# Performance work log

Measured on AMD Instinct MI355X. Metric: run time of the kernel, lower is better.

Reference implementation:

```python
import jax, jax.numpy as jnp
import numpy as np

D_MODEL, N_HEADS, E_LAYERS, D_FF, FACTOR, REP = 128, 8, 5, 64, 3, 128


def setup_inputs() -> dict:
    key = jax.random.key(0)
    ks = jax.random.split(key, 8)
    B, L = 8, 4096
    s = 0.02
    E = E_LAYERS
    def p(k, shape):
        return jax.random.normal(k, shape, jnp.float32) * s
    return dict(
        x=jax.random.normal(ks[0], (B, D_MODEL, L), jnp.float32),
        Wq=p(ks[1], (E, D_MODEL, D_MODEL)), bq=jnp.zeros((E, D_MODEL), jnp.float32),
        Wk=p(ks[2], (E, D_MODEL, D_MODEL)), bk=jnp.zeros((E, D_MODEL), jnp.float32),
        Wv=p(ks[3], (E, D_MODEL, D_MODEL)), bv=jnp.zeros((E, D_MODEL), jnp.float32),
        Wo=p(ks[4], (E, D_MODEL, D_MODEL)), bo=jnp.zeros((E, D_MODEL), jnp.float32),
        W1=p(ks[5], (E, D_FF, D_MODEL)), b1=jnp.zeros((E, D_FF), jnp.float32),
        W2=p(ks[6], (E, D_MODEL, D_FF)), b2=jnp.zeros((E, D_MODEL), jnp.float32),
        ln1_w=jnp.ones((E, D_MODEL), jnp.float32), ln1_b=jnp.zeros((E, D_MODEL), jnp.float32),
        ln2_w=jnp.ones((E, D_MODEL), jnp.float32), ln2_b=jnp.zeros((E, D_MODEL), jnp.float32),
        lnf_w=jnp.ones((D_MODEL,), jnp.float32), lnf_b=jnp.zeros((D_MODEL,), jnp.float32),
        Wp=p(ks[7], (D_MODEL, REP)), bp=jnp.zeros((REP,), jnp.float32),
    )


def _ln(x, w, b, eps=1e-5):
    m = jnp.mean(x, axis=-1, keepdims=True)
    v = jnp.mean((x - m) ** 2, axis=-1, keepdims=True)
    return (x - m) * jax.lax.rsqrt(v + eps) * w + b


def _prob_attn(Q, K, V, key):
    """ProbSparse self-attention (mask_flag=False). Q,K,V: [B,H,L,Eh]."""
    B, H, L, Eh = Q.shape
    c = min(int(FACTOR * np.ceil(np.log(L))), L)  # U_part == u for self-attn
    # sample c keys per query position (shared across batch/head, like torch.randint)
    idx = jax.random.randint(key, (L, c), 0, L)
    Ks = K[:, :, idx, :]                                   # [B,H,L,c,Eh]
    QKs = jnp.einsum('bhle,bhlue->bhlu', Q, Ks)            # sampled scores
    M = QKs.max(-1) - QKs.sum(-1) / L                      # sparsity measure [B,H,L]
    _, top = jax.lax.top_k(M, c)                           # top-u query indices [B,H,c]
    Qr = jnp.take_along_axis(Q, top[..., None], axis=2)    # [B,H,c,Eh]
    scores = jnp.einsum('bhue,bhke->bhuk', Qr, K) * (1.0 / np.sqrt(Eh))
    attn = jax.nn.softmax(scores, axis=-1)                 # [B,H,c,L]
    upd = jnp.einsum('bhuk,bhke->bhue', attn, V)           # [B,H,c,Eh]
    # lazy context: mean of V for non-selected queries
    ctx = jnp.broadcast_to(V.mean(axis=2, keepdims=True), Q.shape)
    bi = jnp.arange(B)[:, None, None]
    hi = jnp.arange(H)[None, :, None]
    ctx = ctx.at[bi, hi, top].set(upd)
    return ctx


def reference(x, Wq, bq, Wk, bk, Wv, bv, Wo, bo, W1, b1, W2, b2,
              ln1_w, ln1_b, ln2_w, ln2_b, lnf_w, lnf_b, Wp, bp):
    B, _, L = x.shape
    Eh = D_MODEL // N_HEADS
    h = jnp.transpose(x, (0, 2, 1))                        # [B,L,D]
    base = jax.random.key(42)
    for l in range(E_LAYERS):
        q = (h @ Wq[l].T + bq[l]).reshape(B, L, N_HEADS, Eh).transpose(0, 2, 1, 3)
        k = (h @ Wk[l].T + bk[l]).reshape(B, L, N_HEADS, Eh).transpose(0, 2, 1, 3)
        v = (h @ Wv[l].T + bv[l]).reshape(B, L, N_HEADS, Eh).transpose(0, 2, 1, 3)
        ctx = _prob_attn(q, k, v, jax.random.fold_in(base, l))
        ctx = ctx.transpose(0, 2, 1, 3).reshape(B, L, D_MODEL)
        h = h + (ctx @ Wo[l].T + bo[l])                    # residual (dropout off)
        h = _ln(h, ln1_w[l], ln1_b[l])
        # 1x1 conv FFN == per-token linear
        y = jax.nn.gelu(h @ W1[l].T + b1[l], approximate=False)
        y = y @ W2[l].T + b2[l]
        h = _ln(h + y, ln2_w[l], ln2_b[l])
    h = _ln(h, lnf_w, lnf_b)
    out = h @ Wp + bp                                      # [B,L,REP]
    return jnp.transpose(out, (0, 2, 1))                   # [B,REP,L]
```

## Files before the change

### kernel.cpp

```cpp
#include <hip/hip_runtime.h>
#include <stdint.h>
#include <math.h>

#define DM   128
#define NH   8
#define EHD  16
#define NLAY 5
#define DFF  64
#define NREP 128
#define NB   8
#define SL   4096
#define NC   27
#define NBH  (NB*NH)
#define NROWS (NB*SL)
#define ACH  4

typedef _Float16 f16;
typedef f16 f16x8 __attribute__((ext_vector_type(8)));
typedef float f32x16 __attribute__((ext_vector_type(16)));

__device__ __forceinline__ uint32_t rotl32(uint32_t v, int d) {
  return (v << d) | (v >> (32 - d));
}

__device__ __forceinline__ void tf2x32(uint32_t k0, uint32_t k1,
                                       uint32_t x0, uint32_t x1,
                                       uint32_t &o0, uint32_t &o1) {
  uint32_t ks2 = k0 ^ k1 ^ 0x1BD11BDAu;
  x0 += k0; x1 += k1;
#define TFR(r) { x0 += x1; x1 = rotl32(x1, (r)); x1 ^= x0; }
  TFR(13) TFR(15) TFR(26) TFR(6)
  x0 += k1; x1 += ks2 + 1u;
  TFR(17) TFR(29) TFR(16) TFR(24)
  x0 += ks2; x1 += k0 + 2u;
  TFR(13) TFR(15) TFR(26) TFR(6)
  x0 += k0; x1 += k1 + 3u;
  TFR(17) TFR(29) TFR(16) TFR(24)
  x0 += k1; x1 += ks2 + 4u;
  TFR(13) TFR(15) TFR(26) TFR(6)
  x0 += ks2; x1 += k0 + 5u;
#undef TFR
  o0 = x0; o1 = x1;
}

__global__ void gen_bits_kernel(uint32_t* __restrict__ bits, int layer) {
  int i = blockIdx.x * blockDim.x + threadIdx.x;
  if (i >= SL * NC) return;
  uint32_t ka, kb, k2a, k2b, y0, y1;
  tf2x32(0u, 42u, 0u, (uint32_t)layer, ka, kb);
  tf2x32(ka, kb, 0u, 1u, k2a, k2b);
  tf2x32(k2a, k2b, 0u, (uint32_t)i, y0, y1);
  bits[i] = y0 ^ y1;
}

__global__ __launch_bounds__(256) void transpose_x_kernel(const float* __restrict__ x,
                                                          float* __restrict__ h) {
  __shared__ float t[32][33];
  int tid = threadIdx.x;
  int tx = tid & 31, ty = tid >> 5;
  int l0 = blockIdx.x * 32, d0 = blockIdx.y * 32, b = blockIdx.z;
#pragma unroll
  for (int j = 0; j < 4; ++j) {
    int d = d0 + ty + 8 * j;
    t[ty + 8 * j][tx] = x[((size_t)b * DM + d) * SL + l0 + tx];
  }
  __syncthreads();
#pragma unroll
  for (int j = 0; j < 4; ++j) {
    int l = l0 + ty + 8 * j;
    h[((size_t)b * SL + l) * DM + d0 + tx] = t[tx][ty + 8 * j];
  }
}

#define PACK_TOTAL 425984
__global__ __launch_bounds__(256) void prep_weights(
    const float* __restrict__ Wq, const float* __restrict__ Wk,
    const float* __restrict__ Wv, const float* __restrict__ Wo,
    const float* __restrict__ W1, const float* __restrict__ W2,
    const float* __restrict__ Wp, f16* __restrict__ phi) {
  int idx = blockIdx.x * 256 + threadIdx.x;
  if (idx >= PACK_TOTAL) return;
  const float* src; int K, KS16, lsh; int f; bool transp = false;
  if (idx >= 409600) { f = idx - 409600; src = Wp; K = 128; KS16 = 8; lsh = 3; transp = true; }
  else {
    int layer = idx / 81920; int r = idx - layer * 81920;
    if      (r < 16384) { src = Wq + layer * 16384; f = r;         K = 128; KS16 = 8; lsh = 3; }
    else if (r < 32768) { src = Wk + layer * 16384; f = r - 16384; K = 128; KS16 = 8; lsh = 3; }
    else if (r < 49152) { src = Wv + layer * 16384; f = r - 32768; K = 128; KS16 = 8; lsh = 3; }
    else if (r < 65536) { src = Wo + layer * 16384; f = r - 49152; K = 128; KS16 = 8; lsh = 3; }
    else if (r < 73728) { src = W1 + layer * 8192;  f = r - 65536; K = 128; KS16 = 8; lsh = 3; }
    else                { src = W2 + layer * 8192;  f = r - 73728; K = 64;  KS16 = 4; lsh = 2; }
  }
  int j = f & 7, lane = (f >> 3) & 63, rest = f >> 9;
  int ks = rest & (KS16 - 1), nt = rest >> lsh;
  int n = nt * 32 + (lane & 31);
  int kk = ks * 16 + ((lane >> 5) & 1) * 8 + j;
  float x = transp ? src[(size_t)kk * 128 + n] : src[(size_t)n * K + kk];
  phi[idx] = (f16)x;
}

template<int NT32, int KS16, int SRC, int EPI>
__global__ __launch_bounds__(256, 2) void gemm_fused(
    const float* __restrict__ Asrc, const f16* __restrict__ phi,
    const float* __restrict__ bias0, const float* __restrict__ bias1,
    const float* __restrict__ bias2,
    float* out0, float* out1, float* out2,
    const float* __restrict__ gw, const float* __restrict__ gb,
    const float* hres) {
  constexpr int NGW = NT32 / 2;
  constexpr int K = KS16 * 16;
  __shared__ f16x8 Alds[2 * 2 * KS16 * 64];
  __shared__ f16x8 Blds[NT32 * KS16 * 64];
  __shared__ float red[64 * 4];
  int tid = threadIdx.x, lane = tid & 63, wid = tid >> 6;
  int mg = wid >> 1, ng = wid & 1;
  int row0 = blockIdx.x * 64;

  if constexpr (SRC == 0 || SRC == 1) {
    constexpr int OCT = 64 * (K / 8);
    for (int o = tid; o < OCT; o += 256) {
      int row = o / (K / 8);
      int k0 = (o % (K / 8)) * 8;
      float4 f0, f1;
      if constexpr (SRC == 0) {
        const float* s = Asrc + (size_t)(row0 + row) * K + k0;
        f0 = *(const float4*)(s);
        f1 = *(const float4*)(s + 4);
      } else {
        int gr = row0 + row; int bb = gr >> 12, ll = gr & (SL - 1);
        int head = k0 >> 4, e0 = k0 & 15;
        const float* s = Asrc + (((size_t)(bb * NH + head) * SL + ll) * EHD + e0);
        f0 = *(const float4*)(s);
        f1 = *(const float4*)(s + 4);
      }
      f16x8 vh, vl;
      float xs[8] = {f0.x, f0.y, f0.z, f0.w, f1.x, f1.y, f1.z, f1.w};
#pragma unroll
      for (int j = 0; j < 8; ++j) {
        f16 hh = (f16)xs[j];
        vh[j] = hh;
        vl[j] = (f16)(xs[j] - (float)hh);
      }
      int al = (row & 31) | (((k0 >> 3) & 1) << 5);
      int ks = k0 >> 4, mt = row >> 5;
      Alds[((0 * 2 + mt) * KS16 + ks) * 64 + al] = vh;
      Alds[((1 * 2 + mt) * KS16 + ks) * 64 + al] = vl;
    }
  } else {
    int row = tid >> 2, q4 = tid & 3;
    const float* s = Asrc + (size_t)(row0 + row) * 128 + q4 * 32;
    float r[32];
#pragma unroll
    for (int i = 0; i < 8; ++i) {
      float4 f = *(const float4*)(s + 4 * i);
      r[4 * i] = f.x; r[4 * i + 1] = f.y; r[4 * i + 2] = f.z; r[4 * i + 3] = f.w;
    }
    float sm = 0.f, s2 = 0.f;
#pragma unroll
    for (int i = 0; i < 32; ++i) { sm += r[i]; s2 += r[i] * r[i]; }
    sm += __shfl_xor(sm, 1, 4); sm += __shfl_xor(sm, 2, 4);
    s2 += __shfl_xor(s2, 1, 4); s2 += __shfl_xor(s2, 2, 4);
    float mean = sm * (1.f / 128.f);
    float var = s2 * (1.f / 128.f) - mean * mean;
    float rstd = 1.0f / sqrtf(var + 1e-5f);
#pragma unroll
    for (int i = 0; i < 32; ++i) {
      int kk = q4 * 32 + i;
      r[i] = (r[i] - mean) * rstd * gw[kk] + gb[kk];
    }
#pragma unroll
    for (int i = 0; i < 4; ++i) {
      int k0 = q4 * 32 + i * 8;
      f16x8 vh, vl;
#pragma unroll
      for (int j = 0; j < 8; ++j) {
        float x = r[8 * i + j];
        f16 hh = (f16)x;
        vh[j] = hh;
        vl[j] = (f16)(x - (float)hh);
      }
      int al = (row & 31) | (((k0 >> 3) & 1) << 5);
      int ks = k0 >> 4, mt = row >> 5;
      Alds[((0 * 2 + mt) * KS16 + ks) * 64 + al] = vh;
      Alds[((1 * 2 + mt) * KS16 + ks) * 64 + al] = vl;
    }
  }

  constexpr int NMAT = (EPI == 0) ? 3 : 1;
  constexpr int BCNT = NT32 * KS16 * 64;

#define STAGE_B(SRCPTR)                                        \
  {                                                            \
    const float4* bsrc = (const float4*)(SRCPTR);              \
    float4* bdst = (float4*)Blds;                              \
    _Pragma("unroll")                                          \
    for (int i = 0; i < BCNT / 256; ++i) bdst[tid + i * 256] = bsrc[tid + i * 256]; \
  }

#define GEMM_PASS(ASEL)                                                         \
  _Pragma("unroll")                                                             \
  for (int ks = 0; ks < KS16; ++ks) {                                           \
    f16x8 afr = Alds[(((ASEL) * 2 + mg) * KS16 + ks) * 64 + lane];              \
    _Pragma("unroll")                                                           \
    for (int g = 0; g < NGW; ++g) {                                             \
      f16x8 bfr = Blds[((ng * NGW + g) * KS16 + ks) * 64 + lane];               \
      acc[g] = __builtin_amdgcn_mfma_f32_32x32x16_f16(afr, bfr, acc[g], 0, 0, 0); \
    }                                                                           \
  }

  for (int m = 0; m < NMAT; ++m) {
    if (m) __syncthreads();
    STAGE_B(phi + m * 16384)
    __syncthreads();
    f32x16 acc[NGW];
#pragma unroll
    for (int g = 0; g < NGW; ++g)
#pragma unroll
      for (int j = 0; j < 16; ++j) acc[g][j] = 0.f;
    GEMM_PASS(0)
    GEMM_PASS(1)

    int hi4 = 4 * (lane >> 5);
    if constexpr (EPI == 0) {
      const float* bm = (m == 0) ? bias0 : (m == 1) ? bias1 : bias2;
      float* om = (m == 0) ? out0 : (m == 1) ? out1 : out2;
#pragma unroll
      for (int g = 0; g < NGW; ++g) {
        int col = ng * (NGW * 32) + g * 32 + (lane & 31);
        float bv = bm[col];
        int head = col >> 4, e = col & 15;
#pragma unroll
        for (int reg = 0; reg < 16; ++reg) {
          int row_l = (reg & 3) + 8 * (reg >> 2) + hi4;
          int grow = row0 + mg * 32 + row_l;
          int bb = grow >> 12, ll = grow & (SL - 1);
          om[((size_t)(bb * NH + head) * SL + ll) * EHD + e] = acc[g][reg] + bv;
        }
      }
    } else if constexpr (EPI == 3) {
#pragma unroll
      for (int g = 0; g < NGW; ++g) {
        int col = ng * (NGW * 32) + g * 32 + (lane & 31);
        float bv = bias0[col];
#pragma unroll
        for (int reg = 0; reg < 16; ++reg) {
          int row_l = (reg & 3) + 8 * (reg >> 2) + hi4;
          int grow = row0 + mg * 32 + row_l;
          int bb = grow >> 12, ll = grow & (SL - 1);
          out0[((size_t)(bb * NREP + col)) * SL + ll] = acc[g][reg] + bv;
        }
      }
    } else {
      float bv[2], gwv[2], gbv[2];
#pragma unroll
      for (int g = 0; g < NGW; ++g) {
        int col = ng * (NGW * 32) + g * 32 + (lane & 31);
        bv[g] = bias0[col]; gwv[g] = gw[col]; gbv[g] = gb[col];
      }
      float ps[16], pq[16];
#pragma unroll
      for (int reg = 0; reg < 16; ++reg) {
        int row_l = (reg & 3) + 8 * (reg >> 2) + hi4;
        int grow = row0 + mg * 32 + row_l;
        float vsum = 0.f, qsum = 0.f;
#pragma unroll
        for (int g = 0; g < NGW; ++g) {
          int col = ng * (NGW * 32) + g * 32 + (lane & 31);
          float t = acc[g][reg] + bv[g] + hres[(size_t)grow * DM + col];
          acc[g][reg] = t;
          vsum += t; qsum += t * t;
        }
        vsum += __shfl_xor(vsum, 1, 32); qsum += __shfl_xor(qsum, 1, 32);
        vsum += __shfl_xor(vsum, 2, 32); qsum += __shfl_xor(qsum, 2, 32);
        vsum += __shfl_xor(vsum, 4, 32); qsum += __shfl_xor(qsum, 4, 32);
        vsum += __shfl_xor(vsum, 8, 32); qsum += __shfl_xor(qsum, 8, 32);
        vsum += __shfl_xor(vsum, 16, 32); qsum += __shfl_xor(qsum, 16, 32);
        ps[reg] = vsum; pq[reg] = qsum;
      }
      __syncthreads();
      if ((lane & 31) == 0) {
#pragma unroll
        for (int reg = 0; reg < 16; ++reg) {
          int row_l = (reg & 3) + 8 * (reg >> 2) + hi4;
          int rl = mg * 32 + row_l;
          red[rl * 4 + ng * 2 + 0] = ps[reg];
          red[rl * 4 + ng * 2 + 1] = pq[reg];
        }
      }
      __syncthreads();
#pragma unroll
      for (int reg = 0; reg < 16; ++reg) {
        int row_l = (reg & 3) + 8 * (reg >> 2) + hi4;
        int rl = mg * 32 + row_l;
        int grow = row0 + rl;
        float st = red[rl * 4 + 0] + red[rl * 4 + 2];
        float qt = red[rl * 4 + 1] + red[rl * 4 + 3];
        float mean = st * (1.f / 128.f);
        float var = qt * (1.f / 128.f) - mean * mean;
        float rstd = 1.0f / sqrtf(var + 1e-5f);
#pragma unroll
        for (int g = 0; g < NGW; ++g) {
          int col = ng * (NGW * 32) + g * 32 + (lane & 31);
          out0[(size_t)grow * DM + col] = (acc[g][reg] - mean) * rstd * gwv[g] + gbv[g];
        }
      }
    }
  }
#undef STAGE_B
#undef GEMM_PASS
}

__global__ __launch_bounds__(256, 2) void gemm_ffn(
    const float* __restrict__ h,
    const f16* __restrict__ w1hi, const f16* __restrict__ w2hi,
    const float* __restrict__ b1, const float* __restrict__ b2,
    const float* __restrict__ gw, const float* __restrict__ gb,
    float* __restrict__ hout) {
  __shared__ f16x8 AldsH[2 * 2 * 8 * 64];
  __shared__ f16x8 Blds1[2 * 8 * 64];
  __shared__ float ybuf[64 * 64];
  __shared__ float red[64 * 4];
  f16x8* Alds2 = AldsH;
  f16x8* Blds2 = AldsH + 1024;
  int tid = threadIdx.x, lane = tid & 63, wid = tid >> 6;
  int mg = wid >> 1, ng = wid & 1;
  int row0 = blockIdx.x * 64;
  int hi4 = 4 * (lane >> 5);

  for (int o = tid; o < 64 * 16; o += 256) {
    int row = o >> 4;
    int k0 = (o & 15) * 8;
    const float* s = h + (size_t)(row0 + row) * 128 + k0;
    float4 f0 = *(const float4*)(s);
    float4 f1 = *(const float4*)(s + 4);
    f16x8 vh, vl;
    float xs[8] = {f0.x, f0.y, f0.z, f0.w, f1.x, f1.y, f1.z, f1.w};
#pragma unroll
    for (int j = 0; j < 8; ++j) {
      f16 hh = (f16)xs[j];
      vh[j] = hh;
      vl[j] = (f16)(xs[j] - (float)hh);
    }
    int al = (row & 31) | (((k0 >> 3) & 1) << 5);
    int ks = k0 >> 4, mt = row >> 5;
    AldsH[((0 * 2 + mt) * 8 + ks) * 64 + al] = vh;
    AldsH[((1 * 2 + mt) * 8 + ks) * 64 + al] = vl;
  }
  {
    const float4* bsrc = (const float4*)w1hi;
    float4* bdst = (float4*)Blds1;
#pragma unroll
    for (int i = 0; i < 4; ++i) bdst[tid + i * 256] = bsrc[tid + i * 256];
  }
  __syncthreads();
  f32x16 acc1;
#pragma unroll
  for (int j = 0; j < 16; ++j) acc1[j] = 0.f;
#pragma unroll
  for (int asel = 0; asel < 2; ++asel)
#pragma unroll
    for (int ks = 0; ks < 8; ++ks) {
      f16x8 afr = AldsH[((asel * 2 + mg) * 8 + ks) * 64 + lane];
      f16x8 bfr = Blds1[(ng * 8 + ks) * 64 + lane];
      acc1 = __builtin_amdgcn_mfma_f32_32x32x16_f16(afr, bfr, acc1, 0, 0, 0);
    }
  {
    int col = ng * 32 + (lane & 31);
    float bv = b1[col];
    const float is2 = 0.707106781186547524f;
#pragma unroll
    for (int reg = 0; reg < 16; ++reg) {
      int row_l = (reg & 3) + 8 * (reg >> 2) + hi4 + mg * 32;
      float a = acc1[reg] + bv;
      ybuf[row_l * 64 + col] = 0.5f * a * (1.f + erff(a * is2));
    }
  }
  __syncthreads();
  for (int o = tid; o < 64 * 8; o += 256) {
    int row = o >> 3;
    int k0 = (o & 7) * 8;
    f16x8 vh, vl;
#pragma unroll
    for (int j = 0; j < 8; ++j) {
      float x = ybuf[row * 64 + k0 + j];
      f16 hh = (f16)x;
      vh[j] = hh;
      vl[j] = (f16)(x - (float)hh);
    }
    int al = (row & 31) | (((k0 >> 3) & 1) << 5);
    int ks = k0 >> 4, mt = row >> 5;
    Alds2[((0 * 2 + mt) * 4 + ks) * 64 + al] = vh;
    Alds2[((1 * 2 + mt) * 4 + ks) * 64 + al] = vl;
  }
  {
    const float4* bsrc = (const float4*)w2hi;
    float4* bdst = (float4*)Blds2;
#pragma unroll
    for (int i = 0; i < 4; ++i) bdst[tid + i * 256] = bsrc[tid + i * 256];
  }
  __syncthreads();
  f32x16 acc[2];
#pragma unroll
  for (int g = 0; g < 2; ++g)
#pragma unroll
    for (int j = 0; j < 16; ++j) acc[g][j] = 0.f;
#pragma unroll
  for (int asel = 0; asel < 2; ++asel)
#pragma unroll
    for (int ks = 0; ks < 4; ++ks) {
      f16x8 afr = Alds2[((asel * 2 + mg) * 4 + ks) * 64 + lane];
#pragma unroll
      for (int g = 0; g < 2; ++g) {
        f16x8 bfr = Blds2[((ng * 2 + g) * 4 + ks) * 64 + lane];
        acc[g] = __builtin_amdgcn_mfma_f32_32x32x16_f16(afr, bfr, acc[g], 0, 0, 0);
      }
    }
  {
    float bv[2], gwv[2], gbv[2];
#pragma unroll
    for (int g = 0; g < 2; ++g) {
      int col = ng * 64 + g * 32 + (lane & 31);
      bv[g] = b2[col]; gwv[g] = gw[col]; gbv[g] = gb[col];
    }
    float ps[16], pq[16];
#pragma unroll
    for (int reg = 0; reg < 16; ++reg) {
      int row_l = (reg & 3) + 8 * (reg >> 2) + hi4;
      int grow = row0 + mg * 32 + row_l;
      float vsum = 0.f, qsum = 0.f;
#pragma unroll
      for (int g = 0; g < 2; ++g) {
        int col = ng * 64 + g * 32 + (lane & 31);
        float t = acc[g][reg] + bv[g] + h[(size_t)grow * DM + col];
        acc[g][reg] = t;
        vsum += t; qsum += t * t;
      }
      vsum += __shfl_xor(vsum, 1, 32); qsum += __shfl_xor(qsum, 1, 32);
      vsum += __shfl_xor(vsum, 2, 32); qsum += __shfl_xor(qsum, 2, 32);
      vsum += __shfl_xor(vsum, 4, 32); qsum += __shfl_xor(qsum, 4, 32);
      vsum += __shfl_xor(vsum, 8, 32); qsum += __shfl_xor(qsum, 8, 32);
      vsum += __shfl_xor(vsum, 16, 32); qsum += __shfl_xor(qsum, 16, 32);
      ps[reg] = vsum; pq[reg] = qsum;
    }
    __syncthreads();
    if ((lane & 31) == 0) {
#pragma unroll
      for (int reg = 0; reg < 16; ++reg) {
        int row_l = (reg & 3) + 8 * (reg >> 2) + hi4;
        int rl = mg * 32 + row_l;
        red[rl * 4 + ng * 2 + 0] = ps[reg];
        red[rl * 4 + ng * 2 + 1] = pq[reg];
      }
    }
    __syncthreads();
#pragma unroll
    for (int reg = 0; reg < 16; ++reg) {
      int row_l = (reg & 3) + 8 * (reg >> 2) + hi4;
      int rl = mg * 32 + row_l;
      int grow = row0 + rl;
      float st = red[rl * 4 + 0] + red[rl * 4 + 2];
      float qt = red[rl * 4 + 1] + red[rl * 4 + 3];
      float mean = st * (1.f / 128.f);
      float var = qt * (1.f / 128.f) - mean * mean;
      float rstd = 1.0f / sqrtf(var + 1e-5f);
#pragma unroll
      for (int g = 0; g < 2; ++g) {
        int col = ng * 64 + g * 32 + (lane & 31);
        hout[(size_t)grow * DM + col] = (acc[g][reg] - mean) * rstd * gwv[g] + gbv[g];
      }
    }
  }
}

__global__ __launch_bounds__(256) void sampM_kernel(const float* __restrict__ q,
    const float* __restrict__ k, const uint32_t* __restrict__ bits,
    float* __restrict__ M) {
  int tid = threadIdx.x;
  int wave = tid >> 6, lane = tid & 63;
  int bh = blockIdx.x & 63;
  int l = (blockIdx.x >> 6) * 4 + wave;
  int u = lane >> 1;
  bool act = (u < NC);
  int uc = act ? u : 0;
  int ki = (int)(bits[l * NC + uc] & (SL - 1));
  int h8 = (lane & 1) * 8;
  const float* kr = k + ((size_t)bh * SL + ki) * EHD + h8;
  float4 k0 = *(const float4*)(kr);
  float4 k1 = *(const float4*)(kr + 4);
  const float* qr = q + ((size_t)bh * SL + l) * EHD + h8;
  float4 q0 = *(const float4*)(qr);
  float4 q1 = *(const float4*)(qr + 4);
  float s = q0.x*k0.x + q0.y*k0.y + q0.z*k0.z + q0.w*k0.w
          + q1.x*k1.x + q1.y*k1.y + q1.z*k1.z + q1.w*k1.w;
  s += __shfl_xor(s, 1, 64);
  float mval = act ? s : -INFINITY;
  float sval = (act && (lane & 1) == 0) ? s : 0.f;
#pragma unroll
  for (int off = 2; off < 64; off <<= 1) {
    mval = fmaxf(mval, __shfl_xor(mval, off, 64));
    sval += __shfl_xor(sval, off, 64);
  }
  if (lane == 0) M[(size_t)bh * SL + l] = mval - sval * (1.0f / (float)SL);
}

__global__ __launch_bounds__(256) void topk_kernel(const float* __restrict__ M,
                                                   int* __restrict__ top) {
  int bh  = blockIdx.x;
  int tid = threadIdx.x;
  int lane = tid & 63, wave = tid >> 6;
  __shared__ float vals[SL];
  __shared__ float wmax[4];
  __shared__ int   widx[4];
  for (int i = tid; i < SL; i += 256) vals[i] = M[(size_t)bh * SL + i];
  __syncthreads();
  for (int u = 0; u < NC; ++u) {
    float bm = -INFINITY; int bi = SL;
#pragma unroll
    for (int j = 0; j < SL / 256; ++j) {
      int i = tid + j * 256;
      float vv = vals[i];
      if (vv > bm) { bm = vv; bi = i; }
    }
#pragma unroll
    for (int off = 32; off > 0; off >>= 1) {
      float v2 = __shfl_xor(bm, off, 64);
      int   i2 = __shfl_xor(bi, off, 64);
      if (v2 > bm || (v2 == bm && i2 < bi)) { bm = v2; bi = i2; }
    }
    if (lane == 0) { wmax[wave] = bm; widx[wave] = bi; }
    __syncthreads();
    if (tid == 0) {
      float b0 = wmax[0]; int x0 = widx[0];
#pragma unroll
      for (int w = 1; w < 4; ++w) {
        float vw = wmax[w]; int iw = widx[w];
        if (vw > b0 || (vw == b0 && iw < x0)) { b0 = vw; x0 = iw; }
      }
      top[bh * NC + u] = x0;
      vals[x0] = -INFINITY;
    }
    __syncthreads();
  }
}

__global__ __launch_bounds__(256) void vmean_part(const float* __restrict__ v,
                                                  float* __restrict__ partial) {
  int bh = blockIdx.x & 63;
  int chunk = blockIdx.x >> 6;
  int tid = threadIdx.x;
  int e = tid & 15, g = tid >> 4;
  const float* vb = v + ((size_t)bh * SL + chunk * 256) * EHD;
  float s = 0.f;
#pragma unroll
  for (int j = 0; j < 16; ++j) s += vb[(size_t)(j * 16 + g) * EHD + e];
  __shared__ float red[256];
  red[tid] = s; __syncthreads();
  for (int st = 128; st >= 16; st >>= 1) {
    if (tid < st) red[tid] += red[tid + st];
    __syncthreads();
  }
  if (tid < EHD) partial[(bh * 16 + chunk) * EHD + tid] = red[tid];
}

__global__ __launch_bounds__(256) void fillctx_kernel(const float* __restrict__ partial,
                                                      float* __restrict__ ctx) {
  __shared__ float vm[EHD];
  int tid = threadIdx.x;
  int t0 = blockIdx.x * 256;
  int bh = t0 >> 14;
  if (tid < EHD) {
    float s = 0.f;
#pragma unroll
    for (int c = 0; c < 16; ++c) s += partial[(bh * 16 + c) * EHD + tid];
    vm[tid] = s * (1.0f / (float)SL);
  }
  __syncthreads();
  int t = t0 + tid;
  int e0 = (t & 3) * 4;
  *(float4*)(ctx + (size_t)t * 4) = make_float4(vm[e0], vm[e0 + 1], vm[e0 + 2], vm[e0 + 3]);
}

__global__ __launch_bounds__(256) void attn_flash(const float* __restrict__ q,
    const float* __restrict__ k, const float* __restrict__ v,
    const int* __restrict__ top, float* __restrict__ pa) {
  int bh = blockIdx.x & 63, ug = (blockIdx.x >> 6) & 3, chunk = blockIdx.x >> 8;
  int tid = threadIdx.x, wid = tid >> 6, lane = tid & 63;
  int base = ug * 7;
  int nq = (ug < 3) ? 7 : 6;
  bool has0 = (wid < nq);
  bool has1 = (wid + 4 < nq);
  int u0 = base + (has0 ? wid : 0);
  int u1 = base + (has1 ? wid + 4 : 0);
  int qi0 = top[bh * NC + u0];
  int qi1 = top[bh * NC + u1];
  float q0[16], q1[16];
  {
    const float* p0 = q + ((size_t)bh * SL + qi0) * EHD;
    const float* p1 = q + ((size_t)bh * SL + qi1) * EHD;
#pragma unroll
    for (int i = 0; i < 4; ++i) {
      float4 f = *(const float4*)(p0 + 4 * i);
      q0[4*i] = f.x; q0[4*i+1] = f.y; q0[4*i+2] = f.z; q0[4*i+3] = f.w;
      float4 g = *(const float4*)(p1 + 4 * i);
      q1[4*i] = g.x; q1[4*i+1] = g.y; q1[4*i+2] = g.z; q1[4*i+3] = g.w;
    }
  }
  float m0 = -INFINITY, m1 = -INFINITY, l0 = 0.f, l1 = 0.f;
  float a0[16], a1[16];
#pragma unroll
  for (int j = 0; j < 16; ++j) { a0[j] = 0.f; a1[j] = 0.f; }
  const float* kb = k + (size_t)bh * SL * EHD;
  const float* vb = v + (size_t)bh * SL * EHD;
  int row_base = chunk * (SL / ACH);
  for (int t = 0; t < SL / ACH / 64; ++t) {
    int ki = row_base + lane + (t << 6);
    float kr[16], vr[16];
    {
      const float* kp = kb + (size_t)ki * EHD;
      const float* vp = vb + (size_t)ki * EHD;
#pragma unroll
      for (int i = 0; i < 4; ++i) {
        float4 f = *(const float4*)(kp + 4 * i);
        kr[4*i] = f.x; kr[4*i+1] = f.y; kr[4*i+2] = f.z; kr[4*i+3] = f.w;
        float4 g = *(const float4*)(vp + 4 * i);
        vr[4*i] = g.x; vr[4*i+1] = g.y; vr[4*i+2] = g.z; vr[4*i+3] = g.w;
      }
    }
    float s0 = 0.f, s1 = 0.f;
#pragma unroll
    for (int j = 0; j < 16; ++j) { s0 += q0[j] * kr[j]; s1 += q1[j] * kr[j]; }
    s0 *= 0.25f; s1 *= 0.25f;
    {
      float d = s0 - m0;
      float e = expf(-fabsf(d));
      bool gt = d > 0.f;
      float c = gt ? e : 1.f;
      float p = gt ? 1.f : e;
      m0 = gt ? s0 : m0;
      l0 = l0 * c + p;
#pragma unroll
      for (int j = 0; j < 16; ++j) a0[j] = a0[j] * c + p * vr[j];
    }
    {
      float d = s1 - m1;
      float e = expf(-fabsf(d));
      bool gt = d > 0.f;
      float c = gt ? e : 1.f;
      float p = gt ? 1.f : e;
      m1 = gt ? s1 : m1;
      l1 = l1 * c + p;
#pragma unroll
      for (int j = 0; j < 16; ++j) a1[j] = a1[j] * c + p * vr[j];
    }
  }
#pragma unroll
  for (int off = 1; off < 64; off <<= 1) {
    {
      float mo = __shfl_xor(m0, off, 64);
      float lo_ = __shfl_xor(l0, off, 64);
      float mn = fmaxf(m0, mo);
      float cs = expf(m0 - mn), co = expf(mo - mn);
      l0 = l0 * cs + lo_ * co;
#pragma unroll
      for (int j = 0; j < 16; ++j) {
        float ao = __shfl_xor(a0[j], off, 64);
        a0[j] = a0[j] * cs + ao * co;
      }
      m0 = mn;
    }
    {
      float mo = __shfl_xor(m1, off, 64);
      float lo_ = __shfl_xor(l1, off, 64);
      float mn = fmaxf(m1, mo);
      float cs = expf(m1 - mn), co = expf(mo - mn);
      l1 = l1 * cs + lo_ * co;
#pragma unroll
      for (int j = 0; j < 16; ++j) {
        float ao = __shfl_xor(a1[j], off, 64);
        a1[j] = a1[j] * cs + ao * co;
      }
      m1 = mn;
    }
  }
  if (lane == 0 && has0) {
    float* o = pa + ((size_t)(bh * NC + u0) * ACH + chunk) * 18;
    o[0] = m0; o[1] = l0;
#pragma unroll
    for (int j = 0; j < 16; ++j) o[2 + j] = a0[j];
  }
  if (lane == 0 && has1) {
    float* o = pa + ((size_t)(bh * NC + u1) * ACH + chunk) * 18;
    o[0] = m1; o[1] = l1;
#pragma unroll
    for (int j = 0; j < 16; ++j) o[2 + j] = a1[j];
  }
}

__global__ __launch_bounds__(64) void attn_merge(const float* __restrict__ pa,
    const int* __restrict__ top, float* __restrict__ ctx) {
  int bh = blockIdx.x;
  int u = threadIdx.x;
  if (u >= NC) return;
  float m = -INFINITY, L = 0.f;
  float a[16];
#pragma unroll
  for (int j = 0; j < 16; ++j) a[j] = 0.f;
#pragma unroll
  for (int c = 0; c < ACH; ++c) {
    const float* p = pa + ((size_t)(bh * NC + u) * ACH + c) * 18;
    float pm = p[0], pl = p[1];
    float mn = fmaxf(m, pm);
    float cs = expf(m - mn), co = expf(pm - mn);
    L = L * cs + pl * co;
#pragma unroll
    for (int j = 0; j < 16; ++j) a[j] = a[j] * cs + p[2 + j] * co;
    m = mn;
  }
  int qi = top[bh * NC + u];
  float inv = 1.0f / L;
  float* o = ctx + ((size_t)bh * SL + qi) * EHD;
#pragma unroll
  for (int j = 0; j < 16; ++j) o[j] = a[j] * inv;
}

extern "C" void kernel_launch(void* const* d_in, const int* in_sizes, int n_in,
                              void* d_out, int out_size, void* d_ws, size_t ws_size,
                              hipStream_t stream) {
  const float* x   = (const float*)d_in[0];
  const float* Wq  = (const float*)d_in[1];
  const float* bq  = (const float*)d_in[2];
  const float* Wk  = (const float*)d_in[3];
  const float* bk  = (const float*)d_in[4];
  const float* Wv  = (const float*)d_in[5];
  const float* bv  = (const float*)d_in[6];
  const float* Wo  = (const float*)d_in[7];
  const float* bo  = (const float*)d_in[8];
  const float* W1  = (const float*)d_in[9];
  const float* b1  = (const float*)d_in[10];
  const float* W2  = (const float*)d_in[11];
  const float* b2  = (const float*)d_in[12];
  const float* ln1w = (const float*)d_in[13];
  const float* ln1b = (const float*)d_in[14];
  const float* ln2w = (const float*)d_in[15];
  const float* ln2b = (const float*)d_in[16];
  const float* lnfw = (const float*)d_in[17];
  const float* lnfb = (const float*)d_in[18];
  const float* Wp  = (const float*)d_in[19];
  const float* bp  = (const float*)d_in[20];
  float* out = (float*)d_out;

  float* ws = (float*)d_ws;
  float* h     = ws;
  float* q     = ws + 4194304;
  float* k     = ws + 8388608;
  float* v     = ws + 12582912;
  float* ctx   = ws + 16777216;
  float* partial = ws + 20971520;
  float* pa    = ws + 20987904;
  float* M     = ws + 23068672;
  int*   top   = (int*)(ws + 23331840);
  uint32_t* bits = (uint32_t*)(ws + 23333888);
  f16* phi = (f16*)(ws + 23444480);

  transpose_x_kernel<<<dim3(SL / 32, DM / 32, NB), 256, 0, stream>>>(x, h);
  prep_weights<<<(PACK_TOTAL + 255) / 256, 256, 0, stream>>>(
      Wq, Wk, Wv, Wo, W1, W2, Wp, phi);

  for (int l = 0; l < NLAY; ++l) {
    size_t lb = (size_t)l * 81920;
    gen_bits_kernel<<<(SL * NC + 255) / 256, 256, 0, stream>>>(bits, l);
    gemm_fused<4, 8, 0, 0><<<NROWS / 64, 256, 0, stream>>>(
        h, phi + lb, bq + l * DM, bk + l * DM, bv + l * DM,
        q, k, v, nullptr, nullptr, nullptr);
    sampM_kernel<<<NBH * SL / 4, 256, 0, stream>>>(q, k, bits, M);
    topk_kernel<<<NBH, 256, 0, stream>>>(M, top);
    vmean_part<<<NBH * 16, 256, 0, stream>>>(v, partial);
    fillctx_kernel<<<NBH * SL * 4 / 256, 256, 0, stream>>>(partial, ctx);
    attn_flash<<<ACH * 256, 256, 0, stream>>>(q, k, v, top, pa);
    attn_merge<<<NBH, 64, 0, stream>>>(pa, top, ctx);
    gemm_fused<4, 8, 1, 1><<<NROWS / 64, 256, 0, stream>>>(
        ctx, phi + lb + 49152, bo + l * DM, nullptr, nullptr,
        h, nullptr, nullptr, ln1w + l * DM, ln1b + l * DM, h);
    gemm_ffn<<<NROWS / 64, 256, 0, stream>>>(
        h, phi + lb + 65536, phi + lb + 73728,
        b1 + l * DFF, b2 + l * DM, ln2w + l * DM, ln2b + l * DM, h);
  }

  gemm_fused<4, 8, 3, 3><<<NROWS / 64, 256, 0, stream>>>(
      h, phi + 409600, bp, nullptr, nullptr,
      out, nullptr, nullptr, lnfw, lnfb, nullptr);
}
```

Before: 941.1 us.

## Store Q and a K copy position-major so sampling reads all heads coalesced

Result: slower. 986.5 us (+4.8%).

```diff
diff --git a/kernel.cpp b/kernel.cpp
--- a/kernel.cpp
+++ b/kernel.cpp
@@ -104,7 +104,7 @@
     const float* __restrict__ Asrc, const f16* __restrict__ phi,
     const float* __restrict__ bias0, const float* __restrict__ bias1,
     const float* __restrict__ bias2,
-    float* out0, float* out1, float* out2,
+    float* out0, float* out1, float* out2, float* out3,
     const float* __restrict__ gw, const float* __restrict__ gb,
     const float* hres) {
   constexpr int NGW = NT32 / 2;
@@ -234,7 +234,14 @@
           int row_l = (reg & 3) + 8 * (reg >> 2) + hi4;
           int grow = row0 + mg * 32 + row_l;
           int bb = grow >> 12, ll = grow & (SL - 1);
-          om[((size_t)(bb * NH + head) * SL + ll) * EHD + e] = acc[g][reg] + bv;
+          float val = acc[g][reg] + bv;
+          if (m == 0) {
+            om[((size_t)ll * NBH + bb * NH + head) * EHD + e] = val;
+          } else {
+            om[((size_t)(bb * NH + head) * SL + ll) * EHD + e] = val;
+            if (m == 1)
+              out3[((size_t)ll * NBH + bb * NH + head) * EHD + e] = val;
+          }
         }
       }
     } else if constexpr (EPI == 3) {
@@ -472,35 +479,55 @@
   }
 }
 
-__global__ __launch_bounds__(256) void sampM_kernel(const float* __restrict__ q,
-    const float* __restrict__ k, const uint32_t* __restrict__ bits,
+__global__ __launch_bounds__(256) void sampM_kernel(const float* __restrict__ qt,
+    const float* __restrict__ kt, const uint32_t* __restrict__ bits,
     float* __restrict__ M) {
+  __shared__ float smx[4][64];
+  __shared__ float ssm[4][64];
   int tid = threadIdx.x;
-  int wave = tid >> 6, lane = tid & 63;
-  int bh = blockIdx.x & 63;
-  int l = (blockIdx.x >> 6) * 4 + wave;
-  int u = lane >> 1;
-  bool act = (u < NC);
-  int uc = act ? u : 0;
-  int ki = (int)(bits[l * NC + uc] & (SL - 1));
-  int h8 = (lane & 1) * 8;
-  const float* kr = k + ((size_t)bh * SL + ki) * EHD + h8;
-  float4 k0 = *(const float4*)(kr);
-  float4 k1 = *(const float4*)(kr + 4);
-  const float* qr = q + ((size_t)bh * SL + l) * EHD + h8;
-  float4 q0 = *(const float4*)(qr);
+  int uslot = tid >> 6, bh = tid & 63;
+  int l = blockIdx.x;
+  const float* qr = qt + ((size_t)l * NBH + bh) * EHD;
+  float4 q0 = *(const float4*)(qr + 0);
   float4 q1 = *(const float4*)(qr + 4);
-  float s = q0.x*k0.x + q0.y*k0.y + q0.z*k0.z + q0.w*k0.w
-          + q1.x*k1.x + q1.y*k1.y + q1.z*k1.z + q1.w*k1.w;
-  s += __shfl_xor(s, 1, 64);
-  float mval = act ? s : -INFINITY;
-  float sval = (act && (lane & 1) == 0) ? s : 0.f;
-#pragma unroll
-  for (int off = 2; off < 64; off <<= 1) {
-    mval = fmaxf(mval, __shfl_xor(mval, off, 64));
-    sval += __shfl_xor(sval, off, 64);
-  }
-  if (lane == 0) M[(size_t)bh * SL + l] = mval - sval * (1.0f / (float)SL);
+  float4 q2 = *(const float4*)(qr + 8);
+  float4 q3 = *(const float4*)(qr + 12);
+  int ucnt = (uslot < 3) ? 7 : 6;
+  int kidx[7];
+#pragma unroll
+  for (int i = 0; i < 7; ++i) {
+    int u = uslot * 7 + i;
+    kidx[i] = (i < ucnt) ? (int)(bits[l * NC + u] & (SL - 1)) : -1;
+  }
+  float mx = -INFINITY, sm = 0.f;
+#pragma unroll
+  for (int i = 0; i < 7; ++i) {
+    if (kidx[i] >= 0) {
+      const float* kr = kt + ((size_t)kidx[i] * NBH + bh) * EHD;
+      float4 k0 = *(const float4*)(kr + 0);
+      float4 k1 = *(const float4*)(kr + 4);
+      float4 k2 = *(const float4*)(kr + 8);
+      float4 k3 = *(const float4*)(kr + 12);
+      float s = q0.x*k0.x + q0.y*k0.y + q0.z*k0.z + q0.w*k0.w
+              + q1.x*k1.x + q1.y*k1.y + q1.z*k1.z + q1.w*k1.w
+              + q2.x*k2.x + q2.y*k2.y + q2.z*k2.z + q2.w*k2.w
+              + q3.x*k3.x + q3.y*k3.y + q3.z*k3.z + q3.w*k3.w;
+      mx = fmaxf(mx, s);
+      sm += s;
+    }
+  }
+  smx[uslot][bh] = mx;
+  ssm[uslot][bh] = sm;
+  __syncthreads();
+  if (uslot == 0) {
+    float m2 = smx[0][bh], s2 = ssm[0][bh];
+#pragma unroll
+    for (int w = 1; w < 4; ++w) {
+      m2 = fmaxf(m2, smx[w][bh]);
+      s2 += ssm[w][bh];
+    }
+    M[(size_t)bh * SL + l] = m2 - s2 * (1.0f / (float)SL);
+  }
 }
 
 __global__ __launch_bounds__(256) void topk_kernel(const float* __restrict__ M,
@@ -580,7 +607,7 @@
   *(float4*)(ctx + (size_t)t * 4) = make_float4(vm[e0], vm[e0 + 1], vm[e0 + 2], vm[e0 + 3]);
 }
 
-__global__ __launch_bounds__(256) void attn_flash(const float* __restrict__ q,
+__global__ __launch_bounds__(256) void attn_flash(const float* __restrict__ qt,
     const float* __restrict__ k, const float* __restrict__ v,
     const int* __restrict__ top, float* __restrict__ pa) {
   int bh = blockIdx.x & 63, ug = (blockIdx.x >> 6) & 3, chunk = blockIdx.x >> 8;
@@ -595,8 +622,8 @@
   int qi1 = top[bh * NC + u1];
   float q0[16], q1[16];
   {
-    const float* p0 = q + ((size_t)bh * SL + qi0) * EHD;
-    const float* p1 = q + ((size_t)bh * SL + qi1) * EHD;
+    const float* p0 = qt + ((size_t)qi0 * NBH + bh) * EHD;
+    const float* p1 = qt + ((size_t)qi1 * NBH + bh) * EHD;
 #pragma unroll
     for (int i = 0; i < 4; ++i) {
       float4 f = *(const float4*)(p0 + 4 * i);
@@ -751,10 +778,11 @@
 
   float* ws = (float*)d_ws;
   float* h     = ws;
-  float* q     = ws + 4194304;
+  float* qt    = ws + 4194304;
   float* k     = ws + 8388608;
   float* v     = ws + 12582912;
   float* ctx   = ws + 16777216;
+  float* kt    = ctx;
   float* partial = ws + 20971520;
   float* pa    = ws + 20987904;
   float* M     = ws + 23068672;
@@ -771,16 +799,16 @@
     gen_bits_kernel<<<(SL * NC + 255) / 256, 256, 0, stream>>>(bits, l);
     gemm_fused<4, 8, 0, 0><<<NROWS / 64, 256, 0, stream>>>(
         h, phi + lb, bq + l * DM, bk + l * DM, bv + l * DM,
-        q, k, v, nullptr, nullptr, nullptr);
-    sampM_kernel<<<NBH * SL / 4, 256, 0, stream>>>(q, k, bits, M);
+        qt, k, v, kt, nullptr, nullptr, nullptr);
+    sampM_kernel<<<SL, 256, 0, stream>>>(qt, kt, bits, M);
     topk_kernel<<<NBH, 256, 0, stream>>>(M, top);
     vmean_part<<<NBH * 16, 256, 0, stream>>>(v, partial);
     fillctx_kernel<<<NBH * SL * 4 / 256, 256, 0, stream>>>(partial, ctx);
-    attn_flash<<<ACH * 256, 256, 0, stream>>>(q, k, v, top, pa);
+    attn_flash<<<ACH * 256, 256, 0, stream>>>(qt, k, v, top, pa);
     attn_merge<<<NBH, 64, 0, stream>>>(pa, top, ctx);
     gemm_fused<4, 8, 1, 1><<<NROWS / 64, 256, 0, stream>>>(
         ctx, phi + lb + 49152, bo + l * DM, nullptr, nullptr,
-        h, nullptr, nullptr, ln1w + l * DM, ln1b + l * DM, h);
+        h, nullptr, nullptr, nullptr, ln1w + l * DM, ln1b + l * DM, h);
     gemm_ffn<<<NROWS / 64, 256, 0, stream>>>(
         h, phi + lb + 65536, phi + lb + 73728,
         b1 + l * DFF, b2 + l * DM, ln2w + l * DM, ln2b + l * DM, h);
@@ -788,5 +816,5 @@
 
   gemm_fused<4, 8, 3, 3><<<NROWS / 64, 256, 0, stream>>>(
       h, phi + 409600, bp, nullptr, nullptr,
-      out, nullptr, nullptr, lnfw, lnfb, nullptr);
-}
+      out, nullptr, nullptr, nullptr, lnfw, lnfb, nullptr);
+}
```
